# Kernel tuning notes

Hardware: AMD Instinct MI355X
Metric: run time of the kernel (lower is better)

Reference implementation:

```python
import jax, jax.numpy as jnp
import numpy as np

B, N, E = 32, 256, 300   # batch, num hyperedges, word emb size
H, K = 256, 8            # nhidden, nhead
MARGIN = 0.2


def setup_inputs() -> dict:
    key = jax.random.key(0)
    ks = jax.random.split(key, 10)
    s_in = 1.0 / np.sqrt(E)
    s_h = 1.0 / np.sqrt(H)
    s_fc = 1.0 / np.sqrt(H * K)
    return {
        'he_anchor': jax.random.normal(ks[0], (B, N, E), jnp.float32),
        'he_pos': jax.random.normal(ks[1], (B, N, E), jnp.float32),
        'he_neg': jax.random.normal(ks[2], (B, N, E), jnp.float32),
        'W_a2h': jax.random.uniform(ks[3], (H, E), jnp.float32, -s_in, s_in),
        'b_a2h': jax.random.uniform(ks[4], (H,), jnp.float32, -s_in, s_in),
        'W_c2h': jax.random.uniform(ks[5], (H, E), jnp.float32, -s_in, s_in),
        'b_c2h': jax.random.uniform(ks[6], (H,), jnp.float32, -s_in, s_in),
        'W_att': jax.random.uniform(ks[7], (K, H), jnp.float32, -s_h, s_h),
        'b_att': jax.random.uniform(ks[8], (K,), jnp.float32, -s_h, s_h),
        'W_fc': jax.random.uniform(ks[9], (1, H * K), jnp.float32, -s_fc, s_fc),
        'b_fc': jnp.zeros((1,), jnp.float32),
    }


def _score(x, y, W_a2h, b_a2h, W_c2h, b_c2h, W_att, b_att, W_fc, b_fc):
    # a2h / c2h projections, then permute to [B, H, N]
    Aa = jnp.transpose(x @ W_a2h.T + b_a2h, (0, 2, 1))  # [B,H,N]
    Ac = jnp.transpose(y @ W_c2h.T + b_c2h, (0, 2, 1))  # [B,H,M]
    # h2att applied to the outer product Aa[b,h,n]*Ac[b,h,m]; fuse into one einsum
    logits = jnp.einsum('bhn,bhm,kh->bknm', Aa, Ac, W_att) + b_att[None, :, None, None]
    b_, k_, n_, m_ = logits.shape
    att = jax.nn.softmax(logits.reshape(b_, k_, n_ * m_), axis=-1).reshape(b_, k_, n_, m_)
    # per-head bilinear aggregation: out[b,k,h] = sum_{n,m} Aa[b,h,n]*att[b,k,n,m]*Ac[b,h,m]
    t = jnp.einsum('bhn,bknm->bkhm', Aa, att)
    out = jnp.einsum('bkhm,bhm->bkh', t, Ac)
    # torch concat order is head-major: [B, K*H]
    out = out.reshape(b_, k_ * H)
    return out @ W_fc.T + b_fc  # [B,1]


def reference(he_anchor, he_pos, he_neg, W_a2h, b_a2h, W_c2h, b_c2h, W_att, b_att, W_fc, b_fc):
    score_p = _score(he_anchor, he_pos, W_a2h, b_a2h, W_c2h, b_c2h, W_att, b_att, W_fc, b_fc)
    score_n = _score(he_anchor, he_neg, W_a2h, b_a2h, W_c2h, b_c2h, W_att, b_att, W_fc, b_fc)
    loss = jnp.mean(jax.nn.relu(score_n - score_p + MARGIN))
    return loss
```

## Files before the change

kernel.cpp:

```cpp
#include <hip/hip_runtime.h>

#define BB 32
#define NN 256
#define EE 300
#define HH 256
#define KK 8
#define MARGINF 0.2f
#define EP 320

typedef __attribute__((ext_vector_type(8))) short bf16x8;
typedef __attribute__((ext_vector_type(4))) float f32x4;
typedef __attribute__((ext_vector_type(16))) float f32x16;

__device__ inline ushort f2bf(float f) {
  unsigned u = __float_as_uint(f);
  u += 0x7fffu + ((u >> 16) & 1u);
  return (ushort)(u >> 16);
}
__device__ inline float bf2f(ushort s) { return __uint_as_float(((unsigned)s) << 16); }
__device__ inline unsigned cvtpk(float lo, float hi) {
  unsigned r;
  asm("v_cvt_pk_bf16_f32 %0, %1, %2" : "=v"(r) : "v"(lo), "v"(hi));
  return r;
}
__device__ inline void gload_lds16(const ushort* g, ushort* l) {
  __builtin_amdgcn_global_load_lds(
      (const __attribute__((address_space(1))) void*)g,
      (__attribute__((address_space(3))) void*)l, 16, 0, 0);
}

__global__ __launch_bounds__(256) void wconv_kernel(
    const float* __restrict__ Wa, const float* __restrict__ Wc,
    ushort* __restrict__ Wt, unsigned* __restrict__ counter)
{
  const int i = blockIdx.x * 256 + threadIdx.x;
  if (i == 0) counter[0] = 0u;
  const int base = i * 4;
  const int w = base / 81920;
  int r = base - w * 81920;
  const int hb = r / 5120; r -= hb * 5120;
  const int ks = r / 512;  r -= ks * 512;
  const int l = r >> 3, j = r & 7;
  const int h = hb * 16 + (l & 15);
  const int e0 = ks * 32 + (l >> 4) * 8 + j;
  const float* src = w ? Wc : Wa;
  ushort4 o = {0, 0, 0, 0};
  if (e0 < EE) {
    const float4 v = *(const float4*)&src[h * EE + e0];
    o.x = f2bf(v.x); o.y = f2bf(v.y); o.z = f2bf(v.z); o.w = f2bf(v.w);
  }
  *(ushort4*)&Wt[base] = o;
}

__global__ __launch_bounds__(256, 3) void proj_kernel(
    const float* __restrict__ he_a, const float* __restrict__ he_p,
    const float* __restrict__ he_n, const ushort* __restrict__ Wt,
    const float* __restrict__ b_a2h, const float* __restrict__ b_c2h,
    ushort* __restrict__ AT)
{
  const int z = blockIdx.y;
  const int which = z >> 5;
  const int b = z & 31;
  const int nb = blockIdx.x;
  const int n0 = nb * 32;
  const int tid = threadIdx.x;
  const int wv = tid >> 6;
  const int lane = tid & 63;
  const int col = lane & 15;
  const int quad = lane >> 4;

  const float* X = (which == 0 ? he_a : which == 1 ? he_p : he_n) + (size_t)b * NN * EE;
  const ushort* W = Wt + (size_t)(which == 0 ? 0 : 1) * 81920;
  const float* bias = (which == 0 ? b_a2h : b_c2h);

  __shared__ __align__(16) ushort sX[32][328];
  __shared__ __align__(16) ushort tr[32][264];

  {
    const int row = tid >> 3, seg = tid & 7;
    const float* xr = X + (size_t)(n0 + row) * EE;
#pragma unroll
    for (int q = 0; q < 10; q++) {
      const int jj = seg + 8 * q;
      float4 xv = {0.f, 0.f, 0.f, 0.f};
      if (jj < 75) xv = *(const float4*)&xr[4 * jj];
      uint2 p; p.x = cvtpk(xv.x, xv.y); p.y = cvtpk(xv.z, xv.w);
      *(uint2*)&sX[row][4 * jj] = p;
    }
  }
  __syncthreads();

  f32x4 acc[2][4];
#pragma unroll
  for (int nf = 0; nf < 2; nf++)
#pragma unroll
    for (int mb = 0; mb < 4; mb++) acc[nf][mb] = (f32x4){0.f, 0.f, 0.f, 0.f};

#pragma unroll
  for (int ks = 0; ks < 10; ks++) {
    const int off = 32 * ks + 8 * quad;
    const bf16x8 a0 = *(const bf16x8*)&sX[col][off];
    const bf16x8 a1 = *(const bf16x8*)&sX[16 + col][off];
#pragma unroll
    for (int mb = 0; mb < 4; mb++) {
      const bf16x8 w8 = *(const bf16x8*)&W[(4 * wv + mb) * 5120 + ks * 512 + lane * 8];
      acc[0][mb] = __builtin_amdgcn_mfma_f32_16x16x32_bf16(a0, w8, acc[0][mb], 0, 0, 0);
      acc[1][mb] = __builtin_amdgcn_mfma_f32_16x16x32_bf16(a1, w8, acc[1][mb], 0, 0, 0);
    }
  }

#pragma unroll
  for (int nf = 0; nf < 2; nf++)
#pragma unroll
    for (int mb = 0; mb < 4; mb++) {
      const float bi = bias[64 * wv + 16 * mb + col];
#pragma unroll
      for (int r = 0; r < 4; r++)
        tr[16 * nf + 4 * quad + r][64 * wv + 16 * mb + col] = f2bf(acc[nf][mb][r] + bi);
    }
  __syncthreads();
  {
    ushort* dst = AT + (size_t)(which * BB + b) * (NN * HH) + (size_t)nb * 8192;
#pragma unroll
    for (int it = 0; it < 4; it++) {
      const int c = it * 256 + tid;
      const int row = c & 31, hs = (c >> 5) & 1, hb = c >> 6;
      *(uint4*)&dst[c * 8] = *(const uint4*)&tr[row][hb * 16 + hs * 8];
    }
  }
}

__global__ __launch_bounds__(512, 1) void attn_kernel(
    const ushort* __restrict__ AT, const float* __restrict__ Watt,
    const float* __restrict__ Wfc, const float* __restrict__ bfc,
    float* __restrict__ scoresK, unsigned* __restrict__ counter,
    float* __restrict__ out)
{
  const int d = blockIdx.x;
  const int x = d & 7;
  const int j = d >> 3;
  const int grp = x * 8 + (j & 7);
  const int kp = j >> 3;
  const int which = grp >> 5;
  const int b = grp & 31;
  const int tid = threadIdx.x;
  const int wid = tid >> 6;
  const int kh = wid >> 2;
  const int ws = wid & 3;
  const int lane = tid & 63;

  const ushort* Ta = AT + (size_t)b * (NN * HH);
  const ushort* Tc = AT + (size_t)((1 + which) * BB + b) * (NN * HH);

  __shared__ __align__(16) ushort sB[65536];
  __shared__ __align__(16) ushort wkb[2][256];
  __shared__ __align__(16) ushort wfb[2][256];
  __shared__ float red[16];
  __shared__ unsigned isLast;

#pragma unroll
  for (int it = 0; it < 16; it++) {
    const int off = (wid * 16 + it) * 512;
    gload_lds16(Tc + off + lane * 8, &sB[off]);
  }
  {
    const int h = tid & 255, hd = tid >> 8;
    const int kt = 2 * kp + hd;
    wkb[hd][h] = f2bf(Watt[(size_t)kt * HH + h] * 1.44269504089f);
    wfb[hd][h] = f2bf(Wfc[(size_t)kt * HH + h]);
  }
  __syncthreads();

  const ushort* wkp = wkb[kh];
  const ushort* wfp = wfb[kh];

  float num = 0.f, den = 0.f;

#pragma unroll 1
  for (int si = 0; si < 2; si++) {
    const int s = si ^ kh;
    bf16x8 saf[16], gaf[16];
    {
      const ushort* abase = Ta + (4 * s + ws) * 8192 + lane * 8;
#pragma unroll
      for (int ks = 0; ks < 16; ks++) {
        const bf16x8 a = *(const bf16x8*)&abase[ks * 512];
        const int off = 16 * ks + 8 * (lane >> 5);
        const bf16x8 w8 = *(const bf16x8*)&wkp[off];
        const bf16x8 f8 = *(const bf16x8*)&wfp[off];
        union { bf16x8 v; unsigned u[4]; } sv, gv;
#pragma unroll
        for (int jj = 0; jj < 4; jj++) {
          const float a0 = bf2f((ushort)a[2 * jj]), a1 = bf2f((ushort)a[2 * jj + 1]);
          sv.u[jj] = cvtpk(a0 * bf2f((ushort)w8[2 * jj]), a1 * bf2f((ushort)w8[2 * jj + 1]));
          gv.u[jj] = cvtpk(a0 * bf2f((ushort)f8[2 * jj]), a1 * bf2f((ushort)f8[2 * jj + 1]));
        }
        saf[ks] = sv.v; gaf[ks] = gv.v;
      }
    }

    const int rot = (2 * kh + ws) & 3;
    f32x16 aS0 = {0,0,0,0,0,0,0,0,0,0,0,0,0,0,0,0};
    f32x16 aG0 = {0,0,0,0,0,0,0,0,0,0,0,0,0,0,0,0};
    f32x16 aS1 = {0,0,0,0,0,0,0,0,0,0,0,0,0,0,0,0};
    f32x16 aG1 = {0,0,0,0,0,0,0,0,0,0,0,0,0,0,0,0};

#define CLUSTER(AS, AG, MBASE, PS, PG, DOW)                                    \
    AS = (f32x16){0,0,0,0,0,0,0,0,0,0,0,0,0,0,0,0};                           \
    AG = (f32x16){0,0,0,0,0,0,0,0,0,0,0,0,0,0,0,0};                           \
    __builtin_amdgcn_s_setprio(1);                                             \
    _Pragma("unroll")                                                          \
    for (int ks = 0; ks < 16; ks++) {                                          \
      const bf16x8 bv = *(const bf16x8*)&sB[(MBASE) + ks * 512 + lane * 8];    \
      AS = __builtin_amdgcn_mfma_f32_32x32x16_bf16(saf[ks], bv, AS, 0, 0, 0);  \
      AG = __builtin_amdgcn_mfma_f32_32x32x16_bf16(gaf[ks], bv, AG, 0, 0, 0);  \
      if (DOW) { const float p = exp2f(PS[ks]); den += p; num = fmaf(p, PG[ks], num); } \
    }                                                                          \
    __builtin_amdgcn_s_setprio(0);

    {
      const int mb0 = rot * 16384;
      CLUSTER(aS0, aG0, mb0, aS1, aG1, 0)
      CLUSTER(aS1, aG1, mb0 + 8192, aS0, aG0, 1)
    }
#pragma unroll 1
    for (int mi = 1; mi < 4; mi++) {
      const int mbase = ((mi + rot) & 3) * 16384;
      CLUSTER(aS0, aG0, mbase, aS1, aG1, 1)
      CLUSTER(aS1, aG1, mbase + 8192, aS0, aG0, 1)
    }
#undef CLUSTER
#pragma unroll
    for (int r = 0; r < 16; r++) {
      const float p = exp2f(aS1[r]);
      den += p; num = fmaf(p, aG1[r], num);
    }
  }

#pragma unroll
  for (int off = 32; off >= 1; off >>= 1) {
    num += __shfl_xor(num, off);
    den += __shfl_xor(den, off);
  }
  if (lane == 0) { red[wid] = num; red[8 + wid] = den; }
  __syncthreads();
  if (tid == 0) {
    const float n0 = red[0] + red[1] + red[2] + red[3];
    const float d0 = red[8] + red[9] + red[10] + red[11];
    const float n1 = red[4] + red[5] + red[6] + red[7];
    const float d1 = red[12] + red[13] + red[14] + red[15];
    atomicExch(&scoresK[(2 * kp) * 64 + grp], n0 / d0);
    atomicExch(&scoresK[(2 * kp + 1) * 64 + grp], n1 / d1);
    __threadfence();
    isLast = (atomicAdd(counter, 1u) == 255u) ? 1u : 0u;
  }
  __syncthreads();

  if (isLast && tid < 64) {
    float s = bfc[0];
#pragma unroll
    for (int kk = 0; kk < KK; kk++)
      s += atomicAdd(&scoresK[kk * 64 + tid], 0.0f);
    const float other = __shfl(s, tid + 32);
    float v = 0.f;
    if (tid < 32) v = fmaxf(other - s + MARGINF, 0.f);
#pragma unroll
    for (int off = 32; off >= 1; off >>= 1) v += __shfl_xor(v, off);
    if (tid == 0) out[0] = v * (1.0f / 32.0f);
  }
}

extern "C" void kernel_launch(void* const* d_in, const int* in_sizes, int n_in,
                              void* d_out, int out_size, void* d_ws, size_t ws_size,
                              hipStream_t stream) {
  const float* he_a  = (const float*)d_in[0];
  const float* he_p  = (const float*)d_in[1];
  const float* he_n  = (const float*)d_in[2];
  const float* W_a2h = (const float*)d_in[3];
  const float* b_a2h = (const float*)d_in[4];
  const float* W_c2h = (const float*)d_in[5];
  const float* b_c2h = (const float*)d_in[6];
  const float* W_att = (const float*)d_in[7];
  const float* W_fc  = (const float*)d_in[9];
  const float* b_fc  = (const float*)d_in[10];

  ushort* AT = (ushort*)d_ws;
  float* scoresK = (float*)(AT + (size_t)3 * BB * NN * HH);
  ushort* Wt = (ushort*)(scoresK + 512);
  unsigned* counter = (unsigned*)(Wt + (size_t)2 * HH * EP);
  (void)ws_size; (void)in_sizes; (void)n_in; (void)out_size;

  wconv_kernel<<<160, 256, 0, stream>>>(W_a2h, W_c2h, Wt, counter);
  dim3 pg(8, 96);
  proj_kernel<<<pg, 256, 0, stream>>>(he_a, he_p, he_n, Wt, b_a2h, b_c2h, AT);
  attn_kernel<<<256, 512, 0, stream>>>(AT, W_att, W_fc, b_fc, scoresK, counter, (float*)d_out);
}
```

Baseline: 132.8 us.

## Fuse weight conversion, projection and attention into one cooperative kernel

Replaces the three kernel launches (weight conversion, projection, attention) with a single cooperative mega-kernel of 256 blocks that uses grid-wide syncs between phases. This removes inter-kernel launch gaps and tail effects. It also moves the final reduction into the last phase, handled by block 0. The projection now runs with 512-thread blocks at occupancy 1, three tiles per block, so per-phase efficiency may drop, and grid.sync adds its own barrier cost. If the cooperative launch fails, the code falls back to the old three-kernel path.

```diff
diff --git a/kernel.cpp b/kernel.cpp
--- a/kernel.cpp
+++ b/kernel.cpp
@@ -1,4 +1,7 @@
 #include <hip/hip_runtime.h>
+#include <hip/hip_cooperative_groups.h>
+
+namespace cg = cooperative_groups;
 
 #define BB 32
 #define NN 256
@@ -27,6 +30,247 @@
   __builtin_amdgcn_global_load_lds(
       (const __attribute__((address_space(1))) void*)g,
       (__attribute__((address_space(3))) void*)l, 16, 0, 0);
+}
+
+struct SMemP { ushort sX[32][328]; ushort tr[32][264]; };
+struct SMemA { ushort sB[65536]; };
+union SMemU { SMemP p; SMemA a; };
+
+__global__ __launch_bounds__(512, 1) void mega_kernel(
+    const float* __restrict__ he_a, const float* __restrict__ he_p,
+    const float* __restrict__ he_n,
+    const float* __restrict__ Wa, const float* __restrict__ b_a2h,
+    const float* __restrict__ Wc, const float* __restrict__ b_c2h,
+    const float* __restrict__ Watt, const float* __restrict__ Wfc,
+    const float* __restrict__ bfc,
+    ushort* __restrict__ AT, float* __restrict__ scoresK,
+    ushort* __restrict__ Wt, float* __restrict__ out)
+{
+  const int d = blockIdx.x;
+  const int tid = threadIdx.x;
+  const int wid = tid >> 6;
+  const int lane = tid & 63;
+  const int col = lane & 15;
+  const int quad = lane >> 4;
+
+  const int x = d & 7;
+  const int j = d >> 3;
+  const int grp = x * 8 + (j & 7);
+  const int kp = j >> 3;
+  const int whichA = grp >> 5;
+  const int bA = grp & 31;
+  const int kh = wid >> 2;
+  const int ws = wid & 3;
+
+  __shared__ __align__(16) SMemU smem;
+  __shared__ __align__(16) ushort wkb[2][256];
+  __shared__ __align__(16) ushort wfb[2][256];
+  __shared__ float red[16];
+
+  cg::grid_group grid = cg::this_grid();
+
+  {
+    const int h = tid & 255, hd = tid >> 8;
+    const int kt = 2 * kp + hd;
+    wkb[hd][h] = f2bf(Watt[(size_t)kt * HH + h] * 1.44269504089f);
+    wfb[hd][h] = f2bf(Wfc[(size_t)kt * HH + h]);
+  }
+
+  {
+    const int id = d * 512 + tid;
+    if (id < 40960) {
+      const int base = id * 4;
+      const int w = base / 81920;
+      int r = base - w * 81920;
+      const int hb = r / 5120; r -= hb * 5120;
+      const int ksq = r / 512; r -= ksq * 512;
+      const int l = r >> 3, jq = r & 7;
+      const int h = hb * 16 + (l & 15);
+      const int e0 = ksq * 32 + (l >> 4) * 8 + jq;
+      const float* src = w ? Wc : Wa;
+      ushort4 o = {0, 0, 0, 0};
+      if (e0 < EE) {
+        const float4 v = *(const float4*)&src[h * EE + e0];
+        o.x = f2bf(v.x); o.y = f2bf(v.y); o.z = f2bf(v.z); o.w = f2bf(v.w);
+      }
+      *(ushort4*)&Wt[base] = o;
+    }
+  }
+  grid.sync();
+
+#pragma unroll 1
+  for (int t = 0; t < 3; t++) {
+    const int tile = 3 * d + t;
+    const int z = tile >> 3, nb = tile & 7;
+    const int whichP = z >> 5, bP = z & 31, n0 = nb * 32;
+    const float* X = (whichP == 0 ? he_a : whichP == 1 ? he_p : he_n)
+                     + (size_t)bP * NN * EE;
+    const ushort* W = Wt + (size_t)(whichP ? 1 : 0) * 81920;
+    const float* bias = (whichP == 0 ? b_a2h : b_c2h);
+
+    {
+      const int row = tid >> 4, seg = tid & 15;
+      const float* xr = X + (size_t)(n0 + row) * EE;
+#pragma unroll
+      for (int q = 0; q < 5; q++) {
+        const int jj = seg + 16 * q;
+        float4 xv = {0.f, 0.f, 0.f, 0.f};
+        if (jj < 75) xv = *(const float4*)&xr[4 * jj];
+        uint2 p; p.x = cvtpk(xv.x, xv.y); p.y = cvtpk(xv.z, xv.w);
+        *(uint2*)&smem.p.sX[row][4 * jj] = p;
+      }
+    }
+    __syncthreads();
+
+    f32x4 acc[2][2];
+#pragma unroll
+    for (int nf = 0; nf < 2; nf++)
+#pragma unroll
+      for (int mb = 0; mb < 2; mb++) acc[nf][mb] = (f32x4){0.f, 0.f, 0.f, 0.f};
+
+#pragma unroll
+    for (int ks = 0; ks < 10; ks++) {
+      const int off = 32 * ks + 8 * quad;
+      const bf16x8 a0 = *(const bf16x8*)&smem.p.sX[col][off];
+      const bf16x8 a1 = *(const bf16x8*)&smem.p.sX[16 + col][off];
+#pragma unroll
+      for (int mb = 0; mb < 2; mb++) {
+        const bf16x8 w8 = *(const bf16x8*)&W[(size_t)(2 * wid + mb) * 5120 + ks * 512 + lane * 8];
+        acc[0][mb] = __builtin_amdgcn_mfma_f32_16x16x32_bf16(a0, w8, acc[0][mb], 0, 0, 0);
+        acc[1][mb] = __builtin_amdgcn_mfma_f32_16x16x32_bf16(a1, w8, acc[1][mb], 0, 0, 0);
+      }
+    }
+
+#pragma unroll
+    for (int nf = 0; nf < 2; nf++)
+#pragma unroll
+      for (int mb = 0; mb < 2; mb++) {
+        const float bi = bias[32 * wid + 16 * mb + col];
+#pragma unroll
+        for (int r = 0; r < 4; r++)
+          smem.p.tr[16 * nf + 4 * quad + r][32 * wid + 16 * mb + col] = f2bf(acc[nf][mb][r] + bi);
+      }
+    __syncthreads();
+    {
+      ushort* dst = AT + (size_t)z * (NN * HH) + (size_t)nb * 8192;
+#pragma unroll
+      for (int it = 0; it < 2; it++) {
+        const int c = it * 512 + tid;
+        const int row = c & 31, hs = (c >> 5) & 1, hb = c >> 6;
+        *(uint4*)&dst[c * 8] = *(const uint4*)&smem.p.tr[row][hb * 16 + hs * 8];
+      }
+    }
+    __syncthreads();
+  }
+  __threadfence();
+  grid.sync();
+
+  const ushort* Ta = AT + (size_t)bA * (NN * HH);
+  const ushort* Tc = AT + (size_t)((1 + whichA) * BB + bA) * (NN * HH);
+
+#pragma unroll
+  for (int it = 0; it < 16; it++) {
+    const int off = (wid * 16 + it) * 512;
+    gload_lds16(Tc + off + lane * 8, &smem.a.sB[off]);
+  }
+
+  const ushort* wkp = wkb[kh];
+  const ushort* wfp = wfb[kh];
+  const ushort* sBp = smem.a.sB;
+
+  float num = 0.f, den = 0.f;
+  {
+    bool first = true;
+#pragma unroll 1
+    for (int si = 0; si < 2; si++) {
+      const int s = si ^ kh;
+      bf16x8 saf[16], gaf[16];
+      {
+        const ushort* abase = Ta + (4 * s + ws) * 8192 + lane * 8;
+#pragma unroll
+        for (int ks = 0; ks < 16; ks++) {
+          const bf16x8 a = *(const bf16x8*)&abase[ks * 512];
+          const int off = 16 * ks + 8 * (lane >> 5);
+          const bf16x8 w8 = *(const bf16x8*)&wkp[off];
+          const bf16x8 f8 = *(const bf16x8*)&wfp[off];
+          union { bf16x8 v; unsigned u[4]; } sv, gv;
+#pragma unroll
+          for (int jj = 0; jj < 4; jj++) {
+            const float a0 = bf2f((ushort)a[2 * jj]), a1 = bf2f((ushort)a[2 * jj + 1]);
+            sv.u[jj] = cvtpk(a0 * bf2f((ushort)w8[2 * jj]), a1 * bf2f((ushort)w8[2 * jj + 1]));
+            gv.u[jj] = cvtpk(a0 * bf2f((ushort)f8[2 * jj]), a1 * bf2f((ushort)f8[2 * jj + 1]));
+          }
+          saf[ks] = sv.v; gaf[ks] = gv.v;
+        }
+      }
+      if (first) { __syncthreads(); first = false; }
+
+      const int rot = (2 * kh + ws) & 3;
+      f32x16 aS0 = {0,0,0,0,0,0,0,0,0,0,0,0,0,0,0,0};
+      f32x16 aG0 = {0,0,0,0,0,0,0,0,0,0,0,0,0,0,0,0};
+      f32x16 aS1 = {0,0,0,0,0,0,0,0,0,0,0,0,0,0,0,0};
+      f32x16 aG1 = {0,0,0,0,0,0,0,0,0,0,0,0,0,0,0,0};
+
+#define CLUSTER(AS, AG, MBASE, PS, PG, DOW)                                    \
+      AS = (f32x16){0,0,0,0,0,0,0,0,0,0,0,0,0,0,0,0};                         \
+      AG = (f32x16){0,0,0,0,0,0,0,0,0,0,0,0,0,0,0,0};                         \
+      __builtin_amdgcn_s_setprio(1);                                           \
+      _Pragma("unroll")                                                        \
+      for (int ks = 0; ks < 16; ks++) {                                        \
+        const bf16x8 bv = *(const bf16x8*)&sBp[(MBASE) + ks * 512 + lane * 8]; \
+        AS = __builtin_amdgcn_mfma_f32_32x32x16_bf16(saf[ks], bv, AS, 0, 0, 0);\
+        AG = __builtin_amdgcn_mfma_f32_32x32x16_bf16(gaf[ks], bv, AG, 0, 0, 0);\
+        if (DOW) { const float p = exp2f(PS[ks]); den += p; num = fmaf(p, PG[ks], num); } \
+      }                                                                        \
+      __builtin_amdgcn_s_setprio(0);
+
+      {
+        const int mb0 = rot * 16384;
+        CLUSTER(aS0, aG0, mb0, aS1, aG1, 0)
+        CLUSTER(aS1, aG1, mb0 + 8192, aS0, aG0, 1)
+      }
+#pragma unroll 1
+      for (int mi = 1; mi < 4; mi++) {
+        const int mbase = ((mi + rot) & 3) * 16384;
+        CLUSTER(aS0, aG0, mbase, aS1, aG1, 1)
+        CLUSTER(aS1, aG1, mbase + 8192, aS0, aG0, 1)
+      }
+#undef CLUSTER
+#pragma unroll
+      for (int r = 0; r < 16; r++) {
+        const float p = exp2f(aS1[r]);
+        den += p; num = fmaf(p, aG1[r], num);
+      }
+    }
+  }
+
+#pragma unroll
+  for (int off = 32; off >= 1; off >>= 1) {
+    num += __shfl_xor(num, off);
+    den += __shfl_xor(den, off);
+  }
+  if (lane == 0) { red[wid] = num; red[8 + wid] = den; }
+  __syncthreads();
+  if (tid == 0) {
+    scoresK[(2 * kp) * 64 + grp] = (red[0] + red[1] + red[2] + red[3]) /
+                                   (red[8] + red[9] + red[10] + red[11]);
+    scoresK[(2 * kp + 1) * 64 + grp] = (red[4] + red[5] + red[6] + red[7]) /
+                                       (red[12] + red[13] + red[14] + red[15]);
+  }
+  __threadfence();
+  grid.sync();
+
+  if (d == 0 && tid < 64) {
+    float s = bfc[0];
+#pragma unroll
+    for (int kk = 0; kk < KK; kk++) s += scoresK[kk * 64 + tid];
+    const float other = __shfl(s, tid + 32);
+    float v = 0.f;
+    if (tid < 32) v = fmaxf(other - s + MARGINF, 0.f);
+#pragma unroll
+    for (int off = 32; off >= 1; off >>= 1) v += __shfl_xor(v, off);
+    if (tid == 0) out[0] = v * (1.0f / 32.0f);
+  }
 }
 
 __global__ __launch_bounds__(256) void wconv_kernel(
@@ -40,9 +284,9 @@
   int r = base - w * 81920;
   const int hb = r / 5120; r -= hb * 5120;
   const int ks = r / 512;  r -= ks * 512;
-  const int l = r >> 3, j = r & 7;
+  const int l = r >> 3, jq = r & 7;
   const int h = hb * 16 + (l & 15);
-  const int e0 = ks * 32 + (l >> 4) * 8 + j;
+  const int e0 = ks * 32 + (l >> 4) * 8 + jq;
   const float* src = w ? Wc : Wa;
   ushort4 o = {0, 0, 0, 0};
   if (e0 < EE) {
@@ -288,10 +532,21 @@
   float* scoresK = (float*)(AT + (size_t)3 * BB * NN * HH);
   ushort* Wt = (ushort*)(scoresK + 512);
   unsigned* counter = (unsigned*)(Wt + (size_t)2 * HH * EP);
+  float* outp = (float*)d_out;
   (void)ws_size; (void)in_sizes; (void)n_in; (void)out_size;
 
-  wconv_kernel<<<160, 256, 0, stream>>>(W_a2h, W_c2h, Wt, counter);
-  dim3 pg(8, 96);
-  proj_kernel<<<pg, 256, 0, stream>>>(he_a, he_p, he_n, Wt, b_a2h, b_c2h, AT);
-  attn_kernel<<<256, 512, 0, stream>>>(AT, W_att, W_fc, b_fc, scoresK, counter, (float*)d_out);
-}
+  void* args[] = {
+    (void*)&he_a, (void*)&he_p, (void*)&he_n,
+    (void*)&W_a2h, (void*)&b_a2h, (void*)&W_c2h, (void*)&b_c2h,
+    (void*)&W_att, (void*)&W_fc, (void*)&b_fc,
+    (void*)&AT, (void*)&scoresK, (void*)&Wt, (void*)&outp
+  };
+  hipError_t err = hipLaunchCooperativeKernel(
+      reinterpret_cast<void*>(mega_kernel), dim3(256), dim3(512), args, 0, stream);
+  if (err != hipSuccess) {
+    wconv_kernel<<<160, 256, 0, stream>>>(W_a2h, W_c2h, Wt, counter);
+    dim3 pg(8, 96);
+    proj_kernel<<<pg, 256, 0, stream>>>(he_a, he_p, he_n, Wt, b_a2h, b_c2h, AT);
+    attn_kernel<<<256, 512, 0, stream>>>(AT, W_att, W_fc, b_fc, scoresK, counter, outp);
+  }
+}
```

Measured after the change: 302.2 us. 128% more time.
